# Kernel optimization log

Hardware: AMD Instinct MI355X
Metric: run time of the kernel (lower is better)

Reference implementation:

```python
import jax, jax.numpy as jnp
import numpy as np

B, C, H, W, D = 2, 256, 40, 40, 40
HEADS = 8


def _conv1x1(x, w, b):
    # 1x1x1 Conv3d == pointwise channel mix: x [B,C,H,W,D], w [O,C], b [O]
    return jnp.einsum('bchwd,oc->bohwd', x, w) + b[None, :, None, None, None]


def setup_inputs() -> dict:
    key = jax.random.key(0)
    ks = jax.random.split(key, 9)
    s = 1.0 / np.sqrt(C)
    return {
        'x': jax.random.normal(ks[0], (B, C, H, W, D), dtype=jnp.float32),
        'wq': jax.random.normal(ks[1], (C, C), dtype=jnp.float32) * s,
        'bq': jax.random.normal(ks[2], (C,), dtype=jnp.float32) * 0.01,
        'wk': jax.random.normal(ks[3], (C, C), dtype=jnp.float32) * s,
        'bk': jax.random.normal(ks[4], (C,), dtype=jnp.float32) * 0.01,
        'wv': jax.random.normal(ks[5], (C, C), dtype=jnp.float32) * s,
        'bv': jax.random.normal(ks[6], (C,), dtype=jnp.float32) * 0.01,
        'wp': jax.random.normal(ks[7], (C, C), dtype=jnp.float32) * s,
        'bp': jax.random.normal(ks[8], (C,), dtype=jnp.float32) * 0.01,
    }


def reference(x, wq, bq, wk, bk, wv, bv, wp, bp):
    b, ch, h, w, d = x.shape
    heads = HEADS
    hd = ch // heads
    scale = hd ** -0.5
    # q/k/v projections are identical across the three branches -> compute once
    q = _conv1x1(x, wq, bq)
    k = _conv1x1(x, wk, bk)
    v = _conv1x1(x, wv, bv)

    def branch(s1, s2, s3):
        # row-major reshape, exactly matching torch .view semantics
        qh = q.reshape(b, heads, hd, s1, s2, s3)
        kh = k.reshape(b, heads, hd, s1, s2, s3)
        vh = v.reshape(b, heads, hd, s1, s2, s3)
        # matmul over last two axes: attend along s2 with s3 as feature dim
        attn = jax.nn.softmax(qh @ jnp.swapaxes(kh, -1, -2) * scale, axis=-1)
        return (attn @ vh).reshape(b, ch, h, w, d)

    out = branch(h, w, d) + branch(w, h, d) + branch(d, h, w)
    return _conv1x1(out, wp, bp)
```

## Files before the change

kernel.cpp:

```cpp
#include <hip/hip_runtime.h>

#define NB 2
#define NC 256
#define NHH 40
#define NSP 64000
#define PL 1600
#define SCALE 0.17677669529663687f

typedef unsigned short u16;
typedef unsigned int   u32;

typedef __attribute__((ext_vector_type(8))) short bf16x8;
typedef __attribute__((ext_vector_type(4))) float f32x4;

__device__ __forceinline__ float bf2f(u16 u) {
    union { u32 i; float f; } c; c.i = ((u32)u) << 16; return c.f;
}
__device__ __forceinline__ u16 f2bf(float f) {
    union { u32 i; float f; } c; c.f = f; u32 x = c.i;
    return (u16)((x + 0x7fffu + ((x >> 16) & 1u)) >> 16);
}
__device__ __forceinline__ u32 pack2(float a, float b) {
    return (u32)f2bf(a) | ((u32)f2bf(b) << 16);
}
__device__ __forceinline__ f32x4 zero4() {
    f32x4 z; z[0] = 0.f; z[1] = 0.f; z[2] = 0.f; z[3] = 0.f; return z;
}
__device__ __forceinline__ bf16x8 zero8() {
    bf16x8 z;
#pragma unroll
    for (int e = 0; e < 8; ++e) z[e] = 0;
    return z;
}

__global__ __launch_bounds__(256) void wfrag3(
    const float* __restrict__ wq, const float* __restrict__ wk,
    const float* __restrict__ wv, u16* __restrict__ dst)
{
    const int gid  = blockIdx.x * 256 + threadIdx.x;
    const int lane = gid & 63;
    const int i    = (gid >> 6) & 1;
    const int wid  = (gid >> 7) & 7;
    const int step = gid >> 10;
    const int m    = step >> 3;
    const int kc   = step & 7;
    const int row  = wid * 32 + i * 16 + (lane & 15);
    const int col  = kc * 32 + ((lane >> 4) << 3);
    const float* s = ((m == 0) ? wq : ((m == 1) ? wk : wv)) + (size_t)row * NC + col;
    const float4 a = *(const float4*)(s);
    const float4 b = *(const float4*)(s + 4);
    ushort4 p0, p1;
    p0.x = f2bf(a.x); p0.y = f2bf(a.y); p0.z = f2bf(a.z); p0.w = f2bf(a.w);
    p1.x = f2bf(b.x); p1.y = f2bf(b.y); p1.z = f2bf(b.z); p1.w = f2bf(b.w);
    u16* d = dst + (size_t)gid * 8;
    *(ushort4*)(d)     = p0;
    *(ushort4*)(d + 4) = p1;
}

__global__ __launch_bounds__(256) void wfrag1(
    const float* __restrict__ w, u16* __restrict__ dst)
{
    const int gid  = blockIdx.x * 256 + threadIdx.x;
    const int lane = gid & 63;
    const int i    = (gid >> 6) & 1;
    const int wid  = (gid >> 7) & 7;
    const int step = (gid >> 10) & 7;
    const int row  = wid * 32 + i * 16 + (lane & 15);
    const int col  = step * 32 + ((lane >> 4) << 3);
    const float* s = w + (size_t)row * NC + col;
    const float4 a = *(const float4*)(s);
    const float4 b = *(const float4*)(s + 4);
    ushort4 p0, p1;
    p0.x = f2bf(a.x); p0.y = f2bf(a.y); p0.z = f2bf(a.z); p0.w = f2bf(a.w);
    p1.x = f2bf(b.x); p1.y = f2bf(b.y); p1.z = f2bf(b.z); p1.w = f2bf(b.w);
    u16* d = dst + (size_t)gid * 8;
    *(ushort4*)(d)     = p0;
    *(ushort4*)(d + 4) = p1;
}

__global__ __launch_bounds__(512, 4) void qkv8(
    const float* __restrict__ x, const u16* __restrict__ wf,
    const float* __restrict__ bq, const float* __restrict__ bk,
    const float* __restrict__ bv,
    u16* __restrict__ q, u16* __restrict__ k, u16* __restrict__ v)
{
    const int b    = blockIdx.z;
    const int n0   = blockIdx.x * 64;
    const int t    = threadIdx.x;
    const int lane = t & 63;
    const int wid  = t >> 6;
    const int o0w  = wid * 32;
    const int row  = lane & 15;
    const int kg   = (lane >> 4) << 3;
    const int g4   = (lane >> 4) << 2;

    __shared__ u16 xs[64][264];

    const float* xb = x + (size_t)b * NC * NSP;

    {
        const int p   = t >> 4;
        const int nn  = (t & 15) << 2;
        const int rot = (t >> 1) & 3;
#pragma unroll
        for (int it = 0; it < 4; ++it) {
            const int c = (it * 32 + p) * 2;
            const float4 fa = *(const float4*)(xb + (size_t)c * NSP + n0 + nn);
            const float4 fb = *(const float4*)(xb + (size_t)(c + 1) * NSP + n0 + nn);
            u32 pk[4] = { pack2(fa.x, fb.x), pack2(fa.y, fb.y),
                          pack2(fa.z, fb.z), pack2(fa.w, fb.w) };
#pragma unroll
            for (int kk = 0; kk < 4; ++kk) {
                const int k2 = (kk + rot) & 3;
                *(u32*)&xs[nn + k2][c] = pk[k2];
            }
        }
    }
    __syncthreads();

    const u16* wfb = wf + (size_t)(wid * 2) * 512 + (size_t)lane * 8;

    f32x4 acc[2][4];
#pragma unroll
    for (int i = 0; i < 2; ++i)
#pragma unroll
        for (int j = 0; j < 4; ++j) acc[i][j] = zero4();

    bf16x8 afp[4][2];
    bf16x8 bfp[2][4];
#pragma unroll
    for (int s = 0; s < 3; ++s) {
        const u16* wn = wfb + (size_t)s * 8192;
        afp[s][0] = *(const bf16x8*)(wn);
        afp[s][1] = *(const bf16x8*)(wn + 512);
    }
#pragma unroll
    for (int j = 0; j < 4; ++j)
        bfp[0][j] = *(const bf16x8*)&xs[16 * j + row][kg];

#pragma unroll
    for (int step = 0; step < 24; ++step) {
        const int m  = step >> 3;
        const int kc = step & 7;

        if (step + 3 < 24) {
            const u16* wn = wfb + (size_t)(step + 3) * 8192;
            afp[(step + 3) & 3][0] = *(const bf16x8*)(wn);
            afp[(step + 3) & 3][1] = *(const bf16x8*)(wn + 512);
        }
        if (step + 1 < 24) {
            const int kc1 = (step + 1) & 7;
#pragma unroll
            for (int j = 0; j < 4; ++j)
                bfp[(step + 1) & 1][j] =
                    *(const bf16x8*)&xs[16 * j + row][kc1 * 32 + kg];
        }

#pragma unroll
        for (int i = 0; i < 2; ++i)
#pragma unroll
            for (int j = 0; j < 4; ++j)
                acc[i][j] = __builtin_amdgcn_mfma_f32_16x16x32_bf16(
                    afp[step & 3][i], bfp[step & 1][j], acc[i][j], 0, 0, 0);

        if (kc == 7) {
            u16* op = ((m == 0) ? q : ((m == 1) ? k : v)) + (size_t)b * NC * NSP;
            const float* bm = (m == 0) ? bq : ((m == 1) ? bk : bv);
#pragma unroll
            for (int i = 0; i < 2; ++i) {
#pragma unroll
                for (int r = 0; r < 4; ++r) {
                    const int o = o0w + 16 * i + g4 + r;
                    const float bb = bm[o];
#pragma unroll
                    for (int j = 0; j < 4; ++j) {
                        const int n = n0 + 16 * j + row;
                        op[(size_t)o * NSP + n] = f2bf(acc[i][j][r] + bb);
                    }
                }
            }
#pragma unroll
            for (int i = 0; i < 2; ++i)
#pragma unroll
                for (int j = 0; j < 4; ++j) acc[i][j] = zero4();
        }
    }
}

__global__ __launch_bounds__(64, 4) void attn_mfma(
    const u16* __restrict__ q, const u16* __restrict__ k,
    const u16* __restrict__ v, u16* __restrict__ a)
{
    const int s = blockIdx.x;
    const size_t base = (size_t)s * PL;
    const int l = threadIdx.x & 63;
    const int g = l >> 4;
    const int c = l & 15;

    __shared__ u16 vs[48][56];
    __shared__ u16 ps[48][56];

#pragma unroll
    for (int it = 0; it < 3; ++it) {
        const int t = l + it * 64;
        *(u32*)&vs[t >> 2][40 + ((t & 3) << 1)] = 0u;
    }

#pragma unroll
    for (int it = 0; it < 7; ++it) {
        const int idx = l + it * 64;
        if (idx < 400) {
            const int j = idx / 10, d4 = (idx % 10) << 2;
            const ushort4 vv = *(const ushort4*)(v + base + j * 40 + d4);
            vs[d4 + 0][j] = vv.x; vs[d4 + 1][j] = vv.y;
            vs[d4 + 2][j] = vv.z; vs[d4 + 3][j] = vv.w;
        }
    }

    f32x4 sacc[3][3];
#pragma unroll
    for (int mt = 0; mt < 3; ++mt)
#pragma unroll
        for (int jt = 0; jt < 3; ++jt) sacc[mt][jt] = zero4();

    {
        bf16x8 aq[3], bk0[3];
#pragma unroll
        for (int mt = 0; mt < 3; ++mt)
            aq[mt] = *(const bf16x8*)(q + base + (size_t)(mt * 16 + c) * 40 + g * 8);
#pragma unroll
        for (int jt = 0; jt < 3; ++jt)
            bk0[jt] = *(const bf16x8*)(k + base + (size_t)(jt * 16 + c) * 40 + g * 8);
#pragma unroll
        for (int mt = 0; mt < 3; ++mt)
#pragma unroll
            for (int jt = 0; jt < 3; ++jt)
                sacc[mt][jt] = __builtin_amdgcn_mfma_f32_16x16x32_bf16(
                    aq[mt], bk0[jt], sacc[mt][jt], 0, 0, 0);

        bf16x8 aq1[3], bk1[3];
#pragma unroll
        for (int mt = 0; mt < 3; ++mt)
            aq1[mt] = (g == 0)
                ? *(const bf16x8*)(q + base + (size_t)(mt * 16 + c) * 40 + 32)
                : zero8();
#pragma unroll
        for (int jt = 0; jt < 3; ++jt)
            bk1[jt] = (g == 0)
                ? *(const bf16x8*)(k + base + (size_t)(jt * 16 + c) * 40 + 32)
                : zero8();
#pragma unroll
        for (int mt = 0; mt < 3; ++mt)
#pragma unroll
            for (int jt = 0; jt < 3; ++jt)
                sacc[mt][jt] = __builtin_amdgcn_mfma_f32_16x16x32_bf16(
                    aq1[mt], bk1[jt], sacc[mt][jt], 0, 0, 0);
    }

    const bool val2 = (c < 8);
#pragma unroll
    for (int mt = 0; mt < 3; ++mt) {
#pragma unroll
        for (int r = 0; r < 4; ++r) {
            const float v0 = sacc[mt][0][r];
            const float v1 = sacc[mt][1][r];
            const float v2 = sacc[mt][2][r];
            float mx = fmaxf(fmaxf(v0, v1), val2 ? v2 : -1e30f);
#pragma unroll
            for (int off = 1; off < 16; off <<= 1)
                mx = fmaxf(mx, __shfl_xor(mx, off, 64));
            const float p0 = __expf((v0 - mx) * SCALE);
            const float p1 = __expf((v1 - mx) * SCALE);
            const float p2 = val2 ? __expf((v2 - mx) * SCALE) : 0.f;
            float sum = p0 + p1 + p2;
#pragma unroll
            for (int off = 1; off < 16; off <<= 1)
                sum += __shfl_xor(sum, off, 64);
            const float inv = 3.0f / sum;
            const int ri = mt * 16 + g * 4 + r;
            ps[ri][c]      = f2bf(p0 * inv);
            ps[ri][c + 16] = f2bf(p1 * inv);
            ps[ri][c + 32] = f2bf(p2 * inv);
        }
    }
    __syncthreads();

    f32x4 oacc[3][3];
#pragma unroll
    for (int mt = 0; mt < 3; ++mt)
#pragma unroll
        for (int nt = 0; nt < 3; ++nt) oacc[mt][nt] = zero4();

    {
        bf16x8 pa[3], vb_[3];
#pragma unroll
        for (int mt = 0; mt < 3; ++mt)
            pa[mt] = *(const bf16x8*)&ps[mt * 16 + c][g * 8];
#pragma unroll
        for (int nt = 0; nt < 3; ++nt)
            vb_[nt] = *(const bf16x8*)&vs[nt * 16 + c][g * 8];
#pragma unroll
        for (int mt = 0; mt < 3; ++mt)
#pragma unroll
            for (int nt = 0; nt < 3; ++nt)
                oacc[mt][nt] = __builtin_amdgcn_mfma_f32_16x16x32_bf16(
                    pa[mt], vb_[nt], oacc[mt][nt], 0, 0, 0);

        bf16x8 pa1[3], vb1[3];
#pragma unroll
        for (int mt = 0; mt < 3; ++mt)
            pa1[mt] = (g < 2) ? *(const bf16x8*)&ps[mt * 16 + c][32 + g * 8] : zero8();
#pragma unroll
        for (int nt = 0; nt < 3; ++nt)
            vb1[nt] = (g < 2) ? *(const bf16x8*)&vs[nt * 16 + c][32 + g * 8] : zero8();
#pragma unroll
        for (int mt = 0; mt < 3; ++mt)
#pragma unroll
            for (int nt = 0; nt < 3; ++nt)
                oacc[mt][nt] = __builtin_amdgcn_mfma_f32_16x16x32_bf16(
                    pa1[mt], vb1[nt], oacc[mt][nt], 0, 0, 0);
    }
    __syncthreads();

#pragma unroll
    for (int mt = 0; mt < 3; ++mt) {
        if (mt == 2 && g >= 2) continue;
#pragma unroll
        for (int r = 0; r < 4; ++r) {
            const int ri = mt * 16 + g * 4 + r;
#pragma unroll
            for (int nt = 0; nt < 3; ++nt) {
                if (nt == 2 && c >= 8) continue;
                ps[ri][nt * 16 + c] = f2bf(oacc[mt][nt][r]);
            }
        }
    }
    __syncthreads();

#pragma unroll
    for (int it = 0; it < 7; ++it) {
        const int idx = l + it * 64;
        if (idx < 400) {
            const int i = idx / 10, d4 = (idx % 10) << 2;
            *(ushort4*)(a + base + (size_t)idx * 4) = *(const ushort4*)&ps[i][d4];
        }
    }
}

__global__ __launch_bounds__(512, 4) void proj8(
    const u16* __restrict__ a, const u16* __restrict__ wf,
    const float* __restrict__ bp, float* __restrict__ out)
{
    const int b    = blockIdx.z;
    const int n0   = blockIdx.x * 64;
    const int t    = threadIdx.x;
    const int lane = t & 63;
    const int wid  = t >> 6;
    const int o0w  = wid * 32;
    const int row  = lane & 15;
    const int kg   = (lane >> 4) << 3;
    const int g4   = (lane >> 4) << 2;

    __shared__ u16 xs[64][264];

    const u16* ab = a + (size_t)b * NC * NSP;

    {
        const int p   = t >> 4;
        const int nn  = (t & 15) << 2;
        const int rot = (t >> 1) & 3;
#pragma unroll
        for (int it = 0; it < 4; ++it) {
            const int c = (it * 32 + p) * 2;
            const ushort4 ua = *(const ushort4*)(ab + (size_t)c * NSP + n0 + nn);
            const ushort4 ub = *(const ushort4*)(ab + (size_t)(c + 1) * NSP + n0 + nn);
            u32 pk[4] = { (u32)ua.x | ((u32)ub.x << 16), (u32)ua.y | ((u32)ub.y << 16),
                          (u32)ua.z | ((u32)ub.z << 16), (u32)ua.w | ((u32)ub.w << 16) };
#pragma unroll
            for (int kk = 0; kk < 4; ++kk) {
                const int k2 = (kk + rot) & 3;
                *(u32*)&xs[nn + k2][c] = pk[k2];
            }
        }
    }
    __syncthreads();

    const u16* wfb = wf + (size_t)(wid * 2) * 512 + (size_t)lane * 8;

    f32x4 acc[2][4];
#pragma unroll
    for (int i = 0; i < 2; ++i)
#pragma unroll
        for (int j = 0; j < 4; ++j) acc[i][j] = zero4();

    bf16x8 afp[4][2];
    bf16x8 bfp[2][4];
#pragma unroll
    for (int s = 0; s < 3; ++s) {
        const u16* wn = wfb + (size_t)s * 8192;
        afp[s][0] = *(const bf16x8*)(wn);
        afp[s][1] = *(const bf16x8*)(wn + 512);
    }
#pragma unroll
    for (int j = 0; j < 4; ++j)
        bfp[0][j] = *(const bf16x8*)&xs[16 * j + row][kg];

#pragma unroll
    for (int step = 0; step < 8; ++step) {
        if (step + 3 < 8) {
            const u16* wn = wfb + (size_t)(step + 3) * 8192;
            afp[(step + 3) & 3][0] = *(const bf16x8*)(wn);
            afp[(step + 3) & 3][1] = *(const bf16x8*)(wn + 512);
        }
        if (step + 1 < 8) {
            const int kc1 = step + 1;
#pragma unroll
            for (int j = 0; j < 4; ++j)
                bfp[(step + 1) & 1][j] =
                    *(const bf16x8*)&xs[16 * j + row][kc1 * 32 + kg];
        }

#pragma unroll
        for (int i = 0; i < 2; ++i)
#pragma unroll
            for (int j = 0; j < 4; ++j)
                acc[i][j] = __builtin_amdgcn_mfma_f32_16x16x32_bf16(
                    afp[step & 3][i], bfp[step & 1][j], acc[i][j], 0, 0, 0);
    }

    float* ob = out + (size_t)b * NC * NSP;
#pragma unroll
    for (int i = 0; i < 2; ++i) {
#pragma unroll
        for (int r = 0; r < 4; ++r) {
            const int o = o0w + 16 * i + g4 + r;
            const float bb = bp[o];
#pragma unroll
            for (int j = 0; j < 4; ++j) {
                const int n = n0 + 16 * j + row;
                ob[(size_t)o * NSP + n] = acc[i][j][r] + bb;
            }
        }
    }
}

extern "C" void kernel_launch(void* const* d_in, const int* in_sizes, int n_in,
                              void* d_out, int out_size, void* d_ws, size_t ws_size,
                              hipStream_t stream)
{
    const float* x  = (const float*)d_in[0];
    const float* wq = (const float*)d_in[1];
    const float* bq = (const float*)d_in[2];
    const float* wk = (const float*)d_in[3];
    const float* bk = (const float*)d_in[4];
    const float* wv = (const float*)d_in[5];
    const float* bv = (const float*)d_in[6];
    const float* wp = (const float*)d_in[7];
    const float* bp = (const float*)d_in[8];
    float* out = (float*)d_out;

    const size_t QE = (size_t)NB * NC * NSP;
    u16* qb = (u16*)d_ws;
    u16* kb = qb + QE;
    u16* vb = kb + QE;
    u16* ab = vb + QE;

    u16* wqf = (u16*)d_out;
    u16* wpf = qb;

    wfrag3<<<96, 256, 0, stream>>>(wq, wk, wv, wqf);
    qkv8<<<dim3(NSP / 64, 1, NB), 512, 0, stream>>>(
        x, wqf, bq, bk, bv, qb, kb, vb);
    attn_mfma<<<dim3(NB * NC * NHH), 64, 0, stream>>>(qb, kb, vb, ab);
    wfrag1<<<32, 256, 0, stream>>>(wp, wpf);
    proj8<<<dim3(NSP / 64, 1, NB), 512, 0, stream>>>(ab, wpf, bp, out);
}
```

Baseline: 235.4 us.

## Pre-transpose x to bf16 channel-last buffer before QKV projection

```diff
diff --git a/kernel.cpp b/kernel.cpp
--- a/kernel.cpp
+++ b/kernel.cpp
@@ -78,8 +78,40 @@
     *(ushort4*)(d + 4) = p1;
 }
 
-__global__ __launch_bounds__(512, 4) void qkv8(
-    const float* __restrict__ x, const u16* __restrict__ wf,
+__global__ __launch_bounds__(256) void xcvt(
+    const float* __restrict__ x, u16* __restrict__ xT)
+{
+    const int b  = blockIdx.z;
+    const int c0 = blockIdx.y * 64;
+    const int n0 = blockIdx.x * 64;
+    const int t  = threadIdx.x;
+
+    __shared__ u16 ls[64][72];
+
+    const float* xb = x + (size_t)b * NC * NSP;
+    const int cl = t >> 4;
+    const int nl = (t & 15) << 2;
+
+#pragma unroll
+    for (int it = 0; it < 4; ++it) {
+        const int c = c0 + it * 16 + cl;
+        const float4 f = *(const float4*)(xb + (size_t)c * NSP + n0 + nl);
+        ls[nl + 0][it * 16 + cl] = f2bf(f.x);
+        ls[nl + 1][it * 16 + cl] = f2bf(f.y);
+        ls[nl + 2][it * 16 + cl] = f2bf(f.z);
+        ls[nl + 3][it * 16 + cl] = f2bf(f.w);
+    }
+    __syncthreads();
+
+    const int rw = t >> 2;
+    const int ch = (t & 3) << 1;
+    u16* dst = xT + ((size_t)b * NSP + n0 + rw) * NC + c0;
+    *(bf16x8*)(dst + ch * 8)     = *(const bf16x8*)&ls[rw][ch * 8];
+    *(bf16x8*)(dst + ch * 8 + 8) = *(const bf16x8*)&ls[rw][ch * 8 + 8];
+}
+
+__global__ __launch_bounds__(512, 4) void qkvA(
+    const u16* __restrict__ xT, const u16* __restrict__ wf,
     const float* __restrict__ bq, const float* __restrict__ bk,
     const float* __restrict__ bv,
     u16* __restrict__ q, u16* __restrict__ k, u16* __restrict__ v)
@@ -94,31 +126,8 @@
     const int kg   = (lane >> 4) << 3;
     const int g4   = (lane >> 4) << 2;
 
-    __shared__ u16 xs[64][264];
-
-    const float* xb = x + (size_t)b * NC * NSP;
-
-    {
-        const int p   = t >> 4;
-        const int nn  = (t & 15) << 2;
-        const int rot = (t >> 1) & 3;
-#pragma unroll
-        for (int it = 0; it < 4; ++it) {
-            const int c = (it * 32 + p) * 2;
-            const float4 fa = *(const float4*)(xb + (size_t)c * NSP + n0 + nn);
-            const float4 fb = *(const float4*)(xb + (size_t)(c + 1) * NSP + n0 + nn);
-            u32 pk[4] = { pack2(fa.x, fb.x), pack2(fa.y, fb.y),
-                          pack2(fa.z, fb.z), pack2(fa.w, fb.w) };
-#pragma unroll
-            for (int kk = 0; kk < 4; ++kk) {
-                const int k2 = (kk + rot) & 3;
-                *(u32*)&xs[nn + k2][c] = pk[k2];
-            }
-        }
-    }
-    __syncthreads();
-
     const u16* wfb = wf + (size_t)(wid * 2) * 512 + (size_t)lane * 8;
+    const u16* xtb = xT + ((size_t)b * NSP + n0 + row) * NC + kg;
 
     f32x4 acc[2][4];
 #pragma unroll
@@ -136,7 +145,7 @@
     }
 #pragma unroll
     for (int j = 0; j < 4; ++j)
-        bfp[0][j] = *(const bf16x8*)&xs[16 * j + row][kg];
+        bfp[0][j] = *(const bf16x8*)(xtb + j * 16 * NC);
 
 #pragma unroll
     for (int step = 0; step < 24; ++step) {
@@ -153,7 +162,7 @@
 #pragma unroll
             for (int j = 0; j < 4; ++j)
                 bfp[(step + 1) & 1][j] =
-                    *(const bf16x8*)&xs[16 * j + row][kc1 * 32 + kg];
+                    *(const bf16x8*)(xtb + j * 16 * NC + kc1 * 32);
         }
 
 #pragma unroll
@@ -466,11 +475,13 @@
     u16* ab = vb + QE;
 
     u16* wqf = (u16*)d_out;
+    u16* xTb = (u16*)d_out + (1 << 18);
     u16* wpf = qb;
 
     wfrag3<<<96, 256, 0, stream>>>(wq, wk, wv, wqf);
-    qkv8<<<dim3(NSP / 64, 1, NB), 512, 0, stream>>>(
-        x, wqf, bq, bk, bv, qb, kb, vb);
+    xcvt<<<dim3(NSP / 64, 4, NB), 256, 0, stream>>>(x, xTb);
+    qkvA<<<dim3(NSP / 64, 1, NB), 512, 0, stream>>>(
+        xTb, wqf, bq, bk, bv, qb, kb, vb);
     attn_mfma<<<dim3(NB * NC * NHH), 64, 0, stream>>>(qb, kb, vb, ab);
     wfrag1<<<32, 256, 0, stream>>>(wp, wpf);
     proj8<<<dim3(NSP / 64, 1, NB), 512, 0, stream>>>(ab, wpf, bp, out);
```

After: 372.5 us. 58.2% more time.
